# Kernel tuning notes

Measured on AMD Instinct MI355X. Metric: run time of the kernel, lower is better.

## Reference

```python
import jax, jax.numpy as jnp
import numpy as np

N_NODES = 50000
N_EDGES = 150000
EMB = 64
IN_DIM = 32
LN_EPS = 1e-5


def setup_inputs() -> dict:
    key = jax.random.key(0)
    k1, k2, k3, k4 = jax.random.split(key, 4)
    h = jax.random.normal(k1, (N_NODES, EMB), dtype=jnp.float32)
    edge_attr = jax.random.normal(k2, (N_EDGES, IN_DIM), dtype=jnp.float32)
    edge_index = jax.random.randint(k3, (2, N_EDGES), 0, N_NODES, dtype=jnp.int64)
    # xavier_uniform for [EMB*EMB, IN_DIM] weight
    limit = float(np.sqrt(6.0 / (EMB * EMB + IN_DIM)))
    W = jax.random.uniform(k4, (EMB * EMB, IN_DIM), dtype=jnp.float32,
                           minval=-limit, maxval=limit)
    b = jnp.zeros((EMB * EMB,), dtype=jnp.float32)
    gamma = jnp.ones((EMB,), dtype=jnp.float32)
    beta = jnp.zeros((EMB,), dtype=jnp.float32)
    return {"h": h, "edge_attr": edge_attr, "W": W, "b": b,
            "gamma": gamma, "beta": beta, "edge_index": edge_index}


def reference(h, edge_attr, W, b, gamma, beta, edge_index):
    M = edge_attr.shape[0]
    E = h.shape[1]
    # per-edge transform matrix from edge features: [M, E, E]
    m = (edge_attr @ W.T + b).reshape(M, E, E)
    # gather target-node features and apply per-edge matvec: [M, E]
    h_j = h[edge_index[1]]
    msg = jnp.einsum('mef,mf->me', m, h_j)
    # scatter-add messages to source nodes
    aggr = jax.ops.segment_sum(msg, edge_index[0], num_segments=h.shape[0])
    # residual + LayerNorm
    x = h + aggr
    mu = jnp.mean(x, axis=-1, keepdims=True)
    var = jnp.mean(jnp.square(x - mu), axis=-1, keepdims=True)
    y = (x - mu) * jax.lax.rsqrt(var + LN_EPS)
    return y * gamma + beta
```

## Files before the change

### kernel.cpp

```cpp
#include <hip/hip_runtime.h>
#include <math.h>

#define N_NODES 50000
#define N_EDGES 150000
#define LN_EPS 1e-5f

#define BM 128
#define WM 32

typedef _Float16 f16x8 __attribute__((ext_vector_type(8)));
typedef float    f32x4 __attribute__((ext_vector_type(4)));

__global__ void prep_kernel(const float* __restrict__ W, const float* __restrict__ b,
                            f16x8* __restrict__ WtF) {
    int tid = blockIdx.x * 256 + threadIdx.x;
    if (tid >= 66 * 4 * 64) return;
    int l  = tid & 63;
    int nb = (tid >> 6) & 3;
    int c  = tid >> 8;
    int k0 = (l >> 4) << 3;
    int e  = nb * 16 + (l & 15);
    const float* src = (c < 64) ? &W[(e * 64 + c) * 32 + k0]
                                : &b[e * 64 + (c - 64) * 32 + k0];
    float4 v0 = *(const float4*)src;
    float4 v1 = *(const float4*)(src + 4);
    f16x8 o;
    o[0] = (_Float16)v0.x; o[1] = (_Float16)v0.y; o[2] = (_Float16)v0.z; o[3] = (_Float16)v0.w;
    o[4] = (_Float16)v1.x; o[5] = (_Float16)v1.y; o[6] = (_Float16)v1.z; o[7] = (_Float16)v1.w;
    WtF[tid] = o;
}

__global__ void init_kernel(const float* __restrict__ h, float* __restrict__ out) {
    int tid = blockIdx.x * 256 + threadIdx.x;
    ((float4*)out)[tid] = ((const float4*)h)[tid];
}

__launch_bounds__(256, 4)
__global__ void edge_kernel(const float* __restrict__ ea,
                            const float* __restrict__ h,
                            const int*   __restrict__ ei,
                            const f16x8* __restrict__ WtF,
                            float* __restrict__ out)
{
    __shared__ float s_hj[BM][68];
    __shared__ int   s_src[BM];

    const int t = threadIdx.x;
    const int m_base = blockIdx.x * BM;

    {
        int row  = t >> 1;
        int half = t & 1;
        int gm   = m_base + row;
        if (gm < N_EDGES) {
            if (half == 0) s_src[row] = ei[gm];
            const float4* hr = (const float4*)&h[(size_t)ei[N_EDGES + gm] * 64 + half * 32];
            #pragma unroll
            for (int j = 0; j < 8; ++j)
                *(float4*)&s_hj[row][half * 32 + j * 4] = hr[j];
        } else {
            if (half == 0) s_src[row] = -1;
            float4 z = make_float4(0.f, 0.f, 0.f, 0.f);
            #pragma unroll
            for (int j = 0; j < 8; ++j)
                *(float4*)&s_hj[row][half * 32 + j * 4] = z;
        }
    }

    const int lane = t & 63;
    const int w    = t >> 6;
    const int r16  = lane & 15;
    const int g    = lane >> 4;
    const int k0   = g * 8;
    const int row0 = w * WM;
    const int rA   = row0 + r16;
    const int rB   = row0 + 16 + r16;

    float eareg[2][8];
    #pragma unroll
    for (int a = 0; a < 2; ++a) {
        int gm = m_base + row0 + a * 16 + r16;
        if (gm < N_EDGES) {
            float4 v0 = *(const float4*)&ea[(size_t)gm * 32 + k0];
            float4 v1 = *(const float4*)&ea[(size_t)gm * 32 + k0 + 4];
            eareg[a][0] = v0.x; eareg[a][1] = v0.y; eareg[a][2] = v0.z; eareg[a][3] = v0.w;
            eareg[a][4] = v1.x; eareg[a][5] = v1.y; eareg[a][6] = v1.z; eareg[a][7] = v1.w;
        } else {
            #pragma unroll
            for (int i = 0; i < 8; ++i) eareg[a][i] = 0.f;
        }
    }

    f32x4 acc[2][4];
    #pragma unroll
    for (int a = 0; a < 2; ++a)
        #pragma unroll
        for (int nb = 0; nb < 4; ++nb)
            acc[a][nb] = (f32x4){0.f, 0.f, 0.f, 0.f};

    __syncthreads();

    f16x8 b0[4], b1[4], b2[4];
    #pragma unroll
    for (int nb = 0; nb < 4; ++nb) b0[nb] = WtF[(0 * 4 + nb) * 64 + lane];
    #pragma unroll
    for (int nb = 0; nb < 4; ++nb) b1[nb] = WtF[(1 * 4 + nb) * 64 + lane];
    #pragma unroll
    for (int nb = 0; nb < 4; ++nb) b2[nb] = WtF[(2 * 4 + nb) * 64 + lane];

    float hc0 = s_hj[rA][0];
    float hc1 = s_hj[rB][0];

    auto step = [&](int c, f16x8* bb, bool loadnext) {
        float hn0 = 0.f, hn1 = 0.f;
        if (loadnext) { hn0 = s_hj[rA][c + 1]; hn1 = s_hj[rB][c + 1]; }
        {
            f16x8 va;
            #pragma unroll
            for (int i = 0; i < 4; ++i) {
                auto p = __builtin_amdgcn_cvt_pkrtz(eareg[0][2 * i]     * hc0,
                                                    eareg[0][2 * i + 1] * hc0);
                va[2 * i] = (_Float16)p[0]; va[2 * i + 1] = (_Float16)p[1];
            }
            #pragma unroll
            for (int nb = 0; nb < 4; ++nb)
                acc[0][nb] = __builtin_amdgcn_mfma_f32_16x16x32_f16(va, bb[nb], acc[0][nb], 0, 0, 0);
        }
        {
            f16x8 va;
            #pragma unroll
            for (int i = 0; i < 4; ++i) {
                auto p = __builtin_amdgcn_cvt_pkrtz(eareg[1][2 * i]     * hc1,
                                                    eareg[1][2 * i + 1] * hc1);
                va[2 * i] = (_Float16)p[0]; va[2 * i + 1] = (_Float16)p[1];
            }
            #pragma unroll
            for (int nb = 0; nb < 4; ++nb)
                acc[1][nb] = __builtin_amdgcn_mfma_f32_16x16x32_f16(va, bb[nb], acc[1][nb], 0, 0, 0);
        }
        hc0 = hn0; hc1 = hn1;
    };

    for (int c = 0; c < 63; c += 3) {
        step(c, b0, true);
        #pragma unroll
        for (int nb = 0; nb < 4; ++nb) b0[nb] = WtF[((c + 3) * 4 + nb) * 64 + lane];
        step(c + 1, b1, true);
        #pragma unroll
        for (int nb = 0; nb < 4; ++nb) b1[nb] = WtF[((c + 4) * 4 + nb) * 64 + lane];
        step(c + 2, b2, true);
        #pragma unroll
        for (int nb = 0; nb < 4; ++nb) b2[nb] = WtF[((c + 5) * 4 + nb) * 64 + lane];
    }
    step(63, b0, false);

    {
        f16x8 va;
        #pragma unroll
        for (int i = 0; i < 4; ++i) {
            auto p = __builtin_amdgcn_cvt_pkrtz(s_hj[rA][k0 + 2 * i], s_hj[rA][k0 + 2 * i + 1]);
            va[2 * i] = (_Float16)p[0]; va[2 * i + 1] = (_Float16)p[1];
        }
        #pragma unroll
        for (int nb = 0; nb < 4; ++nb)
            acc[0][nb] = __builtin_amdgcn_mfma_f32_16x16x32_f16(va, b1[nb], acc[0][nb], 0, 0, 0);
        #pragma unroll
        for (int i = 0; i < 4; ++i) {
            auto p = __builtin_amdgcn_cvt_pkrtz(s_hj[rB][k0 + 2 * i], s_hj[rB][k0 + 2 * i + 1]);
            va[2 * i] = (_Float16)p[0]; va[2 * i + 1] = (_Float16)p[1];
        }
        #pragma unroll
        for (int nb = 0; nb < 4; ++nb)
            acc[1][nb] = __builtin_amdgcn_mfma_f32_16x16x32_f16(va, b1[nb], acc[1][nb], 0, 0, 0);
    }
    {
        f16x8 va;
        #pragma unroll
        for (int i = 0; i < 4; ++i) {
            auto p = __builtin_amdgcn_cvt_pkrtz(s_hj[rA][32 + k0 + 2 * i], s_hj[rA][32 + k0 + 2 * i + 1]);
            va[2 * i] = (_Float16)p[0]; va[2 * i + 1] = (_Float16)p[1];
        }
        #pragma unroll
        for (int nb = 0; nb < 4; ++nb)
            acc[0][nb] = __builtin_amdgcn_mfma_f32_16x16x32_f16(va, b2[nb], acc[0][nb], 0, 0, 0);
        #pragma unroll
        for (int i = 0; i < 4; ++i) {
            auto p = __builtin_amdgcn_cvt_pkrtz(s_hj[rB][32 + k0 + 2 * i], s_hj[rB][32 + k0 + 2 * i + 1]);
            va[2 * i] = (_Float16)p[0]; va[2 * i + 1] = (_Float16)p[1];
        }
        #pragma unroll
        for (int nb = 0; nb < 4; ++nb)
            acc[1][nb] = __builtin_amdgcn_mfma_f32_16x16x32_f16(va, b2[nb], acc[1][nb], 0, 0, 0);
    }

    #pragma unroll
    for (int a = 0; a < 2; ++a) {
        #pragma unroll
        for (int r = 0; r < 4; ++r) {
            int srcn = s_src[row0 + a * 16 + g * 4 + r];
            if (srcn >= 0) {
                #pragma unroll
                for (int nb = 0; nb < 4; ++nb)
                    atomicAdd(&out[(size_t)srcn * 64 + nb * 16 + r16], acc[a][nb][r]);
            }
        }
    }
}

__global__ void ln_kernel(const float* __restrict__ gamma, const float* __restrict__ beta,
                          float* __restrict__ out) {
    int row = blockIdx.x * 4 + (threadIdx.x >> 6);
    int lane = threadIdx.x & 63;
    if (row >= N_NODES) return;
    float x = out[row * 64 + lane];
    float s = x;
    #pragma unroll
    for (int o = 32; o; o >>= 1) s += __shfl_xor(s, o);
    float mu = s * (1.0f / 64.0f);
    float d = x - mu;
    float v = d * d;
    #pragma unroll
    for (int o = 32; o; o >>= 1) v += __shfl_xor(v, o);
    float var = v * (1.0f / 64.0f);
    float r = rsqrtf(var + LN_EPS);
    out[row * 64 + lane] = d * r * gamma[lane] + beta[lane];
}

extern "C" void kernel_launch(void* const* d_in, const int* in_sizes, int n_in,
                              void* d_out, int out_size, void* d_ws, size_t ws_size,
                              hipStream_t stream) {
    const float* h     = (const float*)d_in[0];
    const float* ea    = (const float*)d_in[1];
    const float* W     = (const float*)d_in[2];
    const float* b     = (const float*)d_in[3];
    const float* gamma = (const float*)d_in[4];
    const float* beta  = (const float*)d_in[5];
    const int*   ei    = (const int*)d_in[6];
    float* out = (float*)d_out;

    f16x8* WtF = (f16x8*)d_ws;

    prep_kernel<<<66, 256, 0, stream>>>(W, b, WtF);
    init_kernel<<<(N_NODES * 64 / 4 + 255) / 256, 256, 0, stream>>>(h, out);
    edge_kernel<<<(N_EDGES + BM - 1) / BM, 256, 0, stream>>>(ea, h, ei, WtF, out);
    ln_kernel<<<(N_NODES + 3) / 4, 256, 0, stream>>>(gamma, beta, out);
}
```

Baseline: 165.7 us.

## Double edge tile per wave and use packed fp16 products for A operand

Each wave now handles 64 edges (4 MFMA row tiles) instead of 32, so every loaded weight fragment feeds twice as many MFMAs and global weight traffic per edge is halved. Gathered node features are stored in shared memory as fp16, and edge attributes are pre-packed to fp16 pairs, so the per-step A-operand build uses packed half multiplies instead of fp32 multiplies plus conversions. This costs more registers (occupancy hint lowered from 4 to 3 blocks) and computes the edge_attr*h product in fp16 rather than fp32, which slightly reduces precision.

```diff
diff --git a/kernel.cpp b/kernel.cpp
--- a/kernel.cpp
+++ b/kernel.cpp
@@ -5,11 +5,19 @@
 #define N_EDGES 150000
 #define LN_EPS 1e-5f
 
-#define BM 128
-#define WM 32
+#define BM 256
+#define WM 64
 
 typedef _Float16 f16x8 __attribute__((ext_vector_type(8)));
+typedef _Float16 f16x4 __attribute__((ext_vector_type(4)));
+typedef _Float16 f16x2 __attribute__((ext_vector_type(2)));
 typedef float    f32x4 __attribute__((ext_vector_type(4)));
+
+static __device__ __forceinline__ f16x2 pkrtz(float a, float b) {
+    auto p = __builtin_amdgcn_cvt_pkrtz(a, b);
+    f16x2 r; r[0] = (_Float16)p[0]; r[1] = (_Float16)p[1];
+    return r;
+}
 
 __global__ void prep_kernel(const float* __restrict__ W, const float* __restrict__ b,
                             f16x8* __restrict__ WtF) {
@@ -35,35 +43,38 @@
     ((float4*)out)[tid] = ((const float4*)h)[tid];
 }
 
-__launch_bounds__(256, 4)
+__launch_bounds__(256, 3)
 __global__ void edge_kernel(const float* __restrict__ ea,
                             const float* __restrict__ h,
                             const int*   __restrict__ ei,
                             const f16x8* __restrict__ WtF,
                             float* __restrict__ out)
 {
-    __shared__ float s_hj[BM][68];
-    __shared__ int   s_src[BM];
+    __shared__ _Float16 s_hj[BM][68];
+    __shared__ int      s_src[BM];
 
     const int t = threadIdx.x;
     const int m_base = blockIdx.x * BM;
 
     {
-        int row  = t >> 1;
-        int half = t & 1;
-        int gm   = m_base + row;
+        int gm = m_base + t;
         if (gm < N_EDGES) {
-            if (half == 0) s_src[row] = ei[gm];
-            const float4* hr = (const float4*)&h[(size_t)ei[N_EDGES + gm] * 64 + half * 32];
-            #pragma unroll
-            for (int j = 0; j < 8; ++j)
-                *(float4*)&s_hj[row][half * 32 + j * 4] = hr[j];
+            s_src[t] = ei[gm];
+            const float4* hr = (const float4*)&h[(size_t)ei[N_EDGES + gm] * 64];
+            #pragma unroll
+            for (int j = 0; j < 16; ++j) {
+                float4 v = hr[j];
+                f16x2 p0 = pkrtz(v.x, v.y);
+                f16x2 p1 = pkrtz(v.z, v.w);
+                f16x4 o; o[0] = p0[0]; o[1] = p0[1]; o[2] = p1[0]; o[3] = p1[1];
+                *(f16x4*)&s_hj[t][j * 4] = o;
+            }
         } else {
-            if (half == 0) s_src[row] = -1;
-            float4 z = make_float4(0.f, 0.f, 0.f, 0.f);
-            #pragma unroll
-            for (int j = 0; j < 8; ++j)
-                *(float4*)&s_hj[row][half * 32 + j * 4] = z;
+            s_src[t] = -1;
+            f16x4 z = (f16x4){0, 0, 0, 0};
+            #pragma unroll
+            for (int j = 0; j < 16; ++j)
+                *(f16x4*)&s_hj[t][j * 4] = z;
         }
     }
 
@@ -73,27 +84,30 @@
     const int g    = lane >> 4;
     const int k0   = g * 8;
     const int row0 = w * WM;
-    const int rA   = row0 + r16;
-    const int rB   = row0 + 16 + r16;
-
-    float eareg[2][8];
-    #pragma unroll
-    for (int a = 0; a < 2; ++a) {
-        int gm = m_base + row0 + a * 16 + r16;
+    int rows[4];
+    #pragma unroll
+    for (int a = 0; a < 4; ++a) rows[a] = row0 + a * 16 + r16;
+
+    f16x2 eap[4][4];
+    #pragma unroll
+    for (int a = 0; a < 4; ++a) {
+        int gm = m_base + rows[a];
         if (gm < N_EDGES) {
             float4 v0 = *(const float4*)&ea[(size_t)gm * 32 + k0];
             float4 v1 = *(const float4*)&ea[(size_t)gm * 32 + k0 + 4];
-            eareg[a][0] = v0.x; eareg[a][1] = v0.y; eareg[a][2] = v0.z; eareg[a][3] = v0.w;
-            eareg[a][4] = v1.x; eareg[a][5] = v1.y; eareg[a][6] = v1.z; eareg[a][7] = v1.w;
+            eap[a][0] = pkrtz(v0.x, v0.y);
+            eap[a][1] = pkrtz(v0.z, v0.w);
+            eap[a][2] = pkrtz(v1.x, v1.y);
+            eap[a][3] = pkrtz(v1.z, v1.w);
         } else {
             #pragma unroll
-            for (int i = 0; i < 8; ++i) eareg[a][i] = 0.f;
-        }
-    }
-
-    f32x4 acc[2][4];
-    #pragma unroll
-    for (int a = 0; a < 2; ++a)
+            for (int i = 0; i < 4; ++i) eap[a][i] = (f16x2){0, 0};
+        }
+    }
+
+    f32x4 acc[4][4];
+    #pragma unroll
+    for (int a = 0; a < 4; ++a)
         #pragma unroll
         for (int nb = 0; nb < 4; ++nb)
             acc[a][nb] = (f32x4){0.f, 0.f, 0.f, 0.f};
@@ -108,37 +122,32 @@
     #pragma unroll
     for (int nb = 0; nb < 4; ++nb) b2[nb] = WtF[(2 * 4 + nb) * 64 + lane];
 
-    float hc0 = s_hj[rA][0];
-    float hc1 = s_hj[rB][0];
+    _Float16 hc[4];
+    #pragma unroll
+    for (int a = 0; a < 4; ++a) hc[a] = s_hj[rows[a]][0];
 
     auto step = [&](int c, f16x8* bb, bool loadnext) {
-        float hn0 = 0.f, hn1 = 0.f;
-        if (loadnext) { hn0 = s_hj[rA][c + 1]; hn1 = s_hj[rB][c + 1]; }
-        {
+        _Float16 hn[4] = {0, 0, 0, 0};
+        if (loadnext) {
+            #pragma unroll
+            for (int a = 0; a < 4; ++a) hn[a] = s_hj[rows[a]][c + 1];
+        }
+        #pragma unroll
+        for (int a = 0; a < 4; ++a) {
+            f16x2 hs; hs[0] = hc[a]; hs[1] = hc[a];
+            f16x2 p0 = eap[a][0] * hs;
+            f16x2 p1 = eap[a][1] * hs;
+            f16x2 p2 = eap[a][2] * hs;
+            f16x2 p3 = eap[a][3] * hs;
             f16x8 va;
-            #pragma unroll
-            for (int i = 0; i < 4; ++i) {
-                auto p = __builtin_amdgcn_cvt_pkrtz(eareg[0][2 * i]     * hc0,
-                                                    eareg[0][2 * i + 1] * hc0);
-                va[2 * i] = (_Float16)p[0]; va[2 * i + 1] = (_Float16)p[1];
-            }
+            va[0] = p0[0]; va[1] = p0[1]; va[2] = p1[0]; va[3] = p1[1];
+            va[4] = p2[0]; va[5] = p2[1]; va[6] = p3[0]; va[7] = p3[1];
             #pragma unroll
             for (int nb = 0; nb < 4; ++nb)
-                acc[0][nb] = __builtin_amdgcn_mfma_f32_16x16x32_f16(va, bb[nb], acc[0][nb], 0, 0, 0);
-        }
-        {
-            f16x8 va;
-            #pragma unroll
-            for (int i = 0; i < 4; ++i) {
-                auto p = __builtin_amdgcn_cvt_pkrtz(eareg[1][2 * i]     * hc1,
-                                                    eareg[1][2 * i + 1] * hc1);
-                va[2 * i] = (_Float16)p[0]; va[2 * i + 1] = (_Float16)p[1];
-            }
-            #pragma unroll
-            for (int nb = 0; nb < 4; ++nb)
-                acc[1][nb] = __builtin_amdgcn_mfma_f32_16x16x32_f16(va, bb[nb], acc[1][nb], 0, 0, 0);
-        }
-        hc0 = hn0; hc1 = hn1;
+                acc[a][nb] = __builtin_amdgcn_mfma_f32_16x16x32_f16(va, bb[nb], acc[a][nb], 0, 0, 0);
+        }
+        #pragma unroll
+        for (int a = 0; a < 4; ++a) hc[a] = hn[a];
     };
 
     for (int c = 0; c < 63; c += 3) {
@@ -154,47 +163,24 @@
     }
     step(63, b0, false);
 
-    {
-        f16x8 va;
-        #pragma unroll
-        for (int i = 0; i < 4; ++i) {
-            auto p = __builtin_amdgcn_cvt_pkrtz(s_hj[rA][k0 + 2 * i], s_hj[rA][k0 + 2 * i + 1]);
-            va[2 * i] = (_Float16)p[0]; va[2 * i + 1] = (_Float16)p[1];
-        }
-        #pragma unroll
-        for (int nb = 0; nb < 4; ++nb)
-            acc[0][nb] = __builtin_amdgcn_mfma_f32_16x16x32_f16(va, b1[nb], acc[0][nb], 0, 0, 0);
-        #pragma unroll
-        for (int i = 0; i < 4; ++i) {
-            auto p = __builtin_amdgcn_cvt_pkrtz(s_hj[rB][k0 + 2 * i], s_hj[rB][k0 + 2 * i + 1]);
-            va[2 * i] = (_Float16)p[0]; va[2 * i + 1] = (_Float16)p[1];
-        }
-        #pragma unroll
-        for (int nb = 0; nb < 4; ++nb)
-            acc[1][nb] = __builtin_amdgcn_mfma_f32_16x16x32_f16(va, b1[nb], acc[1][nb], 0, 0, 0);
-    }
-    {
-        f16x8 va;
-        #pragma unroll
-        for (int i = 0; i < 4; ++i) {
-            auto p = __builtin_amdgcn_cvt_pkrtz(s_hj[rA][32 + k0 + 2 * i], s_hj[rA][32 + k0 + 2 * i + 1]);
-            va[2 * i] = (_Float16)p[0]; va[2 * i + 1] = (_Float16)p[1];
-        }
-        #pragma unroll
-        for (int nb = 0; nb < 4; ++nb)
-            acc[0][nb] = __builtin_amdgcn_mfma_f32_16x16x32_f16(va, b2[nb], acc[0][nb], 0, 0, 0);
-        #pragma unroll
-        for (int i = 0; i < 4; ++i) {
-            auto p = __builtin_amdgcn_cvt_pkrtz(s_hj[rB][32 + k0 + 2 * i], s_hj[rB][32 + k0 + 2 * i + 1]);
-            va[2 * i] = (_Float16)p[0]; va[2 * i + 1] = (_Float16)p[1];
-        }
-        #pragma unroll
-        for (int nb = 0; nb < 4; ++nb)
-            acc[1][nb] = __builtin_amdgcn_mfma_f32_16x16x32_f16(va, b2[nb], acc[1][nb], 0, 0, 0);
-    }
-
-    #pragma unroll
-    for (int a = 0; a < 2; ++a) {
+    #pragma unroll
+    for (int half = 0; half < 2; ++half) {
+        f16x8* bb = half ? b2 : b1;
+        #pragma unroll
+        for (int a = 0; a < 4; ++a) {
+            f16x4 lo = *(const f16x4*)&s_hj[rows[a]][half * 32 + k0];
+            f16x4 hi = *(const f16x4*)&s_hj[rows[a]][half * 32 + k0 + 4];
+            f16x8 va;
+            va[0] = lo[0]; va[1] = lo[1]; va[2] = lo[2]; va[3] = lo[3];
+            va[4] = hi[0]; va[5] = hi[1]; va[6] = hi[2]; va[7] = hi[3];
+            #pragma unroll
+            for (int nb = 0; nb < 4; ++nb)
+                acc[a][nb] = __builtin_amdgcn_mfma_f32_16x16x32_f16(va, bb[nb], acc[a][nb], 0, 0, 0);
+        }
+    }
+
+    #pragma unroll
+    for (int a = 0; a < 4; ++a) {
         #pragma unroll
         for (int r = 0; r < 4; ++r) {
             int srcn = s_src[row0 + a * 16 + g * 4 + r];
```

After: 158.1 us. 1.05x faster.
